# Optimization experiments

Measured on AMD Instinct MI355X. Metric: run time of the kernel, lower is better.

The kernel has to match this reference:

```python
import jax, jax.numpy as jnp
import numpy as np

N, E = 50000, 800000
DIN, H, R, HEADS, DH, OUT = 256, 128, 8, 8, 16, 3  # DH = H // HEADS


def setup_inputs() -> dict:
    key = jax.random.key(0)
    ks = jax.random.split(key, 16)
    g = lambda k, shape, fan: jax.random.normal(k, shape, jnp.float32) * np.float32(np.sqrt(2.0 / fan))
    return {
        'x': jax.random.normal(ks[0], (N, DIN), jnp.float32),
        'edge_index': jax.random.randint(ks[1], (2, E), 0, N, jnp.int32),
        'edge_type': jax.random.randint(ks[2], (E,), 0, R, jnp.int32),
        'Wp': g(ks[3], (DIN, H), DIN), 'bp': jnp.zeros((H,), jnp.float32),
        'W1': g(ks[4], (R, H, H), H), 'root1': g(ks[5], (H, H), H), 'b1': jnp.zeros((H,), jnp.float32),
        'W2': g(ks[6], (R, H, H), H), 'root2': g(ks[7], (H, H), H), 'b2': jnp.zeros((H,), jnp.float32),
        'Wg': g(ks[8], (H, HEADS * DH), H), 'att': g(ks[9], (1, HEADS, 2 * DH), 2 * DH),
        'bg': jnp.zeros((HEADS * DH,), jnp.float32),
        'Wf': g(ks[10], (H, OUT), H), 'bf': jnp.zeros((OUT,), jnp.float32),
    }


def _rgcn(h, src, tgt, etype, W, root, b):
    # h: [N,H]; per-relation: mean-aggregate W_r @ h_src over edges of type r
    n = h.shape[0]
    h_src = h[src]                                   # [E,H]
    out = h @ root
    for r in range(R):
        mask = (etype == r)
        msg = jnp.where(mask[:, None], h_src @ W[r], 0.0)          # [E,H]
        agg = jax.ops.segment_sum(msg, tgt, num_segments=n)        # [N,H]
        deg = jax.ops.segment_sum(mask.astype(h.dtype), tgt, num_segments=n)
        out = out + agg / jnp.clip(deg, 1.0)[:, None]
    return out + b


def _gat(h, src, tgt, Wg, att, bg, negative_slope=0.2):
    n = h.shape[0]
    z = (h @ Wg).reshape(n, HEADS, DH)               # [N,heads,dh]
    z_src, z_tgt = z[src], z[tgt]                    # [E,heads,dh]
    alpha = (z_src * att[:, :, :DH]).sum(-1) + (z_tgt * att[:, :, DH:]).sum(-1)  # [E,heads]
    alpha = jax.nn.leaky_relu(alpha, negative_slope)
    amax = jax.ops.segment_max(alpha, tgt, num_segments=n)         # [N,heads]
    ex = jnp.exp(alpha - amax[tgt])
    denom = jnp.clip(jax.ops.segment_sum(ex, tgt, num_segments=n), 1e-16)
    alpha = ex / denom[tgt]
    out = jax.ops.segment_sum(z_src * alpha[:, :, None], tgt, num_segments=n)  # [N,heads,dh]
    return out.reshape(n, HEADS * DH) + bg


def reference(x, edge_index, edge_type, Wp, bp, W1, root1, b1, W2, root2, b2, Wg, att, bg, Wf, bf):
    src, tgt = edge_index[0], edge_index[1]
    h = x @ Wp + bp
    h = jax.nn.relu(_rgcn(h, src, tgt, edge_type, W1, root1, b1))
    h = jax.nn.relu(_rgcn(h, src, tgt, edge_type, W2, root2, b2))
    h = _gat(h, src, tgt, Wg, att, bg)
    logits = h @ Wf + bf
    return jax.nn.log_softmax(logits, axis=-1)
```

## Files before the change

kernel.cpp:

```cpp
#include <hip/hip_runtime.h>
#include <math.h>

#define NN      50000
#define EE      800000
#define DIN     256
#define HF      128
#define RR      8
#define NHEADS  8
#define DHH     16
#define OUTC    3
#define M2      (NN * RR)
#define NB2     ((M2 + 255) / 256)
#define CH2     ((NB2 + 255) / 256)

static inline int cdiv(long long a, int b) { return (int)((a + b - 1) / b); }

typedef __attribute__((ext_vector_type(8))) short short8;
typedef __attribute__((ext_vector_type(4))) float f32x4;

__device__ inline float bf2f(unsigned short u) {
    return __uint_as_float(((unsigned)u) << 16);
}
__device__ inline unsigned short f2bf(float f) {
    unsigned u = __float_as_uint(f);
    u += 0x7fffu + ((u >> 16) & 1u);
    return (unsigned short)(u >> 16);
}

__global__ __launch_bounds__(256) void prep_weights(const float* __restrict__ Wp,
                                                    const float* __restrict__ W1,
                                                    const float* __restrict__ root1,
                                                    const float* __restrict__ W2,
                                                    const float* __restrict__ root2,
                                                    const float* __restrict__ Wg,
                                                    unsigned short* __restrict__ Wtp_hi,
                                                    unsigned short* __restrict__ Wtp_lo,
                                                    unsigned short* __restrict__ Wt1_hi,
                                                    unsigned short* __restrict__ Wt1_lo,
                                                    unsigned short* __restrict__ Wt2_hi,
                                                    unsigned short* __restrict__ Wt2_lo,
                                                    unsigned short* __restrict__ Wtg_hi,
                                                    unsigned short* __restrict__ Wtg_lo) {
    int i = blockIdx.x * 256 + threadIdx.x;
    if (i >= 344064) return;
    const float* src; unsigned short *dh, *dl; int k0, ldk, base;
    if (i < 32768)       { src = Wp;    dh = Wtp_hi; dl = Wtp_lo; k0 = 0;    ldk = 256;  base = 0; }
    else if (i < 163840) { src = W1;    dh = Wt1_hi; dl = Wt1_lo; k0 = 0;    ldk = 1152; base = 32768; }
    else if (i < 180224) { src = root1; dh = Wt1_hi; dl = Wt1_lo; k0 = 1024; ldk = 1152; base = 163840; }
    else if (i < 311296) { src = W2;    dh = Wt2_hi; dl = Wt2_lo; k0 = 0;    ldk = 1152; base = 180224; }
    else if (i < 327680) { src = root2; dh = Wt2_hi; dl = Wt2_lo; k0 = 1024; ldk = 1152; base = 311296; }
    else                 { src = Wg;    dh = Wtg_hi; dl = Wtg_lo; k0 = 0;    ldk = 128;  base = 327680; }
    int j = i - base;
    int k = j >> 7, n = j & 127;
    float f = src[(size_t)k * 128 + n];
    unsigned short hi = f2bf(f);
    unsigned short lo = f2bf(f - bf2f(hi));
    dh[(size_t)n * ldk + k0 + k] = hi;
    dl[(size_t)n * ldk + k0 + k] = lo;
}

__global__ __launch_bounds__(256) void count2_kernel(const int* __restrict__ tgt,
                                                     const int* __restrict__ et,
                                                     int* __restrict__ cnt2) {
    int i = blockIdx.x * 256 + threadIdx.x;
    if (i < EE) atomicAdd(&cnt2[tgt[i] * RR + et[i]], 1);
}

__global__ __launch_bounds__(256) void scan1_kernel(const int* __restrict__ cnt,
                                                    int* __restrict__ bsum, int n) {
    __shared__ int s[256];
    int t = threadIdx.x;
    int i = blockIdx.x * 256 + t;
    s[t] = (i < n) ? cnt[i] : 0;
    __syncthreads();
    for (int off = 128; off > 0; off >>= 1) {
        if (t < off) s[t] += s[t + off];
        __syncthreads();
    }
    if (t == 0) bsum[blockIdx.x] = s[0];
// ... 137 lines not shown
        *reinterpret_cast<uint4*>(&Bh[srow * APAD + spart]) = rvbh;
        *reinterpret_cast<uint4*>(&Bl[srow * APAD + spart]) = rvbl;
    };

    const int NT = K / BK;
    load_t(0); write_t(); __syncthreads();
    for (int t = 0; t < NT; t++) {
        if (t + 1 < NT) load_t((t + 1) * BK);

        short8 ah[4], al[4];
#pragma unroll
        for (int tt = 0; tt < 4; tt++) {
            ah[tt] = *reinterpret_cast<const short8*>(&Ah[(wr * 64 + tt * 16 + lrow) * APAD + q * 8]);
            if (SPLITA)
                al[tt] = *reinterpret_cast<const short8*>(&Al[(wr * 64 + tt * 16 + lrow) * APAD + q * 8]);
        }
#pragma unroll
        for (int cc = 0; cc < 2; cc++) {
            int cb = wc * 2 + cc;
            short8 bh = *reinterpret_cast<const short8*>(&Bh[(cb * 16 + lrow) * APAD + q * 8]);
            short8 bl = *reinterpret_cast<const short8*>(&Bl[(cb * 16 + lrow) * APAD + q * 8]);
#pragma unroll
            for (int tt = 0; tt < 4; tt++) {
                acc[tt][cc] = __builtin_amdgcn_mfma_f32_16x16x32_bf16(ah[tt], bl, acc[tt][cc], 0, 0, 0);
                if (SPLITA)
                    acc[tt][cc] = __builtin_amdgcn_mfma_f32_16x16x32_bf16(al[tt], bh, acc[tt][cc], 0, 0, 0);
                acc[tt][cc] = __builtin_amdgcn_mfma_f32_16x16x32_bf16(ah[tt], bh, acc[tt][cc], 0, 0, 0);
            }
        }
        __syncthreads();
        if (t + 1 < NT) { write_t(); __syncthreads(); }
    }

#pragma unroll
    for (int t = 0; t < 4; t++) {
#pragma unroll
        for (int r = 0; r < 4; r++) {
            int gmo = m0 + wr * 64 + t * 16 + q * 4 + r;
            if (gmo >= M) continue;
#pragma unroll
            for (int cc = 0; cc < 2; cc++) {
                int gn = (wc * 2 + cc) * 16 + lrow;
                float v = acc[t][cc][r];
                if (BIAS) v += bias[gn];
                if (ACC)  v += C[(size_t)gmo * HF + gn];
                if (RELU) v = fmaxf(v, 0.f);
                C[(size_t)gmo * HF + gn] = v;
                if (BF16OUT) Cb[(size_t)gmo * HF + gn] = f2bf(v);
            }
        }
    }
}

__global__ __launch_bounds__(512) void gemm_rgcn(const unsigned short* __restrict__ aggb,
                                                 const float* __restrict__ hin,
                                                 const unsigned short* __restrict__ Bthi,
                                                 const unsigned short* __restrict__ Btlo,
                                                 float* __restrict__ hout,
                                                 unsigned short* __restrict__ hbout,
                                                 const float* __restrict__ bias, int M) {
    const int LDK = (RR + 1) * HF;
    __shared__ unsigned short Ah[128 * APAD];
    __shared__ unsigned short Al[128 * APAD];
    __shared__ unsigned short Bh[128 * APAD];
    __shared__ unsigned short Bl[128 * APAD];
    const int tid  = threadIdx.x;
    const int m0   = blockIdx.x * 128;
    const int wr   = (tid >> 6) >> 2;
    const int wc   = (tid >> 6) & 3;
    const int lane = tid & 63;
    const int lrow = lane & 15;
    const int q    = lane >> 4;

    f32x4 acc[4][2];
#pragma unroll
    for (int t = 0; t < 4; t++)
#pragma unroll
        for (int c = 0; c < 2; c++) acc[t][c] = (f32x4){0.f, 0.f, 0.f, 0.f};

    const int srow  = tid >> 2;
    const int spart = (tid & 3) * 8;
    const int gm    = m0 + srow;

    uint4 rva1 = make_uint4(0u, 0u, 0u, 0u);
    float rva2[8];
    uint4 rvbh, rvbl;

    auto load1 = [&](int k0) {
        rva1 = make_uint4(0u, 0u, 0u, 0u);
        if (gm < M) rva1 = *reinterpret_cast<const uint4*>(&aggb[(size_t)gm * (RR * HF) + k0 + spart]);
        rvbh = *reinterpret_cast<const uint4*>(&Bthi[(size_t)srow * LDK + k0 + spart]);
        rvbl = *reinterpret_cast<const uint4*>(&Btlo[(size_t)srow * LDK + k0 + spart]);
    };
    auto write1 = [&]() {
        *reinterpret_cast<uint4*>(&Ah[srow * APAD + spart]) = rva1;
        *reinterpret_cast<uint4*>(&Bh[srow * APAD + spart]) = rvbh;
        *reinterpret_cast<uint4*>(&Bl[srow * APAD + spart]) = rvbl;
    };
    auto load2 = [&](int k0) {
        if (gm < M) {
            const float* ap = &hin[(size_t)gm * HF + k0 + spart];
            float4 v0 = *reinterpret_cast<const float4*>(ap);
            float4 v1 = *reinterpret_cast<const float4*>(ap + 4);
            rva2[0] = v0.x; rva2[1] = v0.y; rva2[2] = v0.z; rva2[3] = v0.w;
            rva2[4] = v1.x; rva2[5] = v1.y; rva2[6] = v1.z; rva2[7] = v1.w;
        } else {
#pragma unroll
            for (int j = 0; j < 8; j++) rva2[j] = 0.f;
        }
        rvbh = *reinterpret_cast<const uint4*>(&Bthi[(size_t)srow * LDK + RR * HF + k0 + spart]);
        rvbl = *reinterpret_cast<const uint4*>(&Btlo[(size_t)srow * LDK + RR * HF + k0 + spart]);
    };
    auto write2 = [&]() {
        unsigned hw[4], lw[4];
#pragma unroll
        for (int j = 0; j < 4; j++) {
            unsigned short h0 = f2bf(rva2[2 * j]);
            unsigned short h1 = f2bf(rva2[2 * j + 1]);
            unsigned short l0 = f2bf(rva2[2 * j] - bf2f(h0));
            unsigned short l1 = f2bf(rva2[2 * j + 1] - bf2f(h1));
            hw[j] = (unsigned)h0 | ((unsigned)h1 << 16);
            lw[j] = (unsigned)l0 | ((unsigned)l1 << 16);
        }
        *reinterpret_cast<uint4*>(&Ah[srow * APAD + spart]) = make_uint4(hw[0], hw[1], hw[2], hw[3]);
        *reinterpret_cast<uint4*>(&Al[srow * APAD + spart]) = make_uint4(lw[0], lw[1], lw[2], lw[3]);
        *reinterpret_cast<uint4*>(&Bh[srow * APAD + spart]) = rvbh;
        *reinterpret_cast<uint4*>(&Bl[srow * APAD + spart]) = rvbl;
    };

    load1(0); write1(); __syncthreads();
    for (int t = 0; t < 32; t++) {
        if (t < 31) load1((t + 1) * BK);
        else        load2(0);

        short8 ah[4];
#pragma unroll
        for (int tt = 0; tt < 4; tt++)
            ah[tt] = *reinterpret_cast<const short8*>(&Ah[(wr * 64 + tt * 16 + lrow) * APAD + q * 8]);
#pragma unroll
        for (int cc = 0; cc < 2; cc++) {
            int cb = wc * 2 + cc;
            short8 bh = *reinterpret_cast<const short8*>(&Bh[(cb * 16 + lrow) * APAD + q * 8]);
            short8 bl = *reinterpret_cast<const short8*>(&Bl[(cb * 16 + lrow) * APAD + q * 8]);
#pragma unroll
            for (int tt = 0; tt < 4; tt++) {
                acc[tt][cc] = __builtin_amdgcn_mfma_f32_16x16x32_bf16(ah[tt], bl, acc[tt][cc], 0, 0, 0);
                acc[tt][cc] = __builtin_amdgcn_mfma_f32_16x16x32_bf16(ah[tt], bh, acc[tt][cc], 0, 0, 0);
            }
        }
        __syncthreads();
        if (t < 31) write1(); else write2();
        __syncthreads();
    }

    for (int t = 0; t < 4; t++) {
        if (t < 3) load2((t + 1) * BK);

        short8 ah[4], al[4];
#pragma unroll
        for (int tt = 0; tt < 4; tt++) {
            ah[tt] = *reinterpret_cast<const short8*>(&Ah[(wr * 64 + tt * 16 + lrow) * APAD + q * 8]);
            al[tt] = *reinterpret_cast<const short8*>(&Al[(wr * 64 + tt * 16 + lrow) * APAD + q * 8]);
        }
#pragma unroll
        for (int cc = 0; cc < 2; cc++) {
            int cb = wc * 2 + cc;
            short8 bh = *reinterpret_cast<const short8*>(&Bh[(cb * 16 + lrow) * APAD + q * 8]);
            short8 bl = *reinterpret_cast<const short8*>(&Bl[(cb * 16 + lrow) * APAD + q * 8]);
#pragma unroll
            for (int tt = 0; tt < 4; tt++) {
                acc[tt][cc] = __builtin_amdgcn_mfma_f32_16x16x32_bf16(ah[tt], bl, acc[tt][cc], 0, 0, 0);
                acc[tt][cc] = __builtin_amdgcn_mfma_f32_16x16x32_bf16(al[tt], bh, acc[tt][cc], 0, 0, 0);
                acc[tt][cc] = __builtin_amdgcn_mfma_f32_16x16x32_bf16(ah[tt], bh, acc[tt][cc], 0, 0, 0);
            }
        }
        if (t < 3) {
            __syncthreads();
            write2();
            __syncthreads();
        }
    }

#pragma unroll
    for (int t = 0; t < 4; t++) {
#pragma unroll
        for (int r = 0; r < 4; r++) {
            int gmo = m0 + wr * 64 + t * 16 + q * 4 + r;
            if (gmo >= M) continue;
#pragma unroll
            for (int cc = 0; cc < 2; cc++) {
                int gn = (wc * 2 + cc) * 16 + lrow;
                float v = fmaxf(acc[t][cc][r] + bias[gn], 0.f);
                hout[(size_t)gmo * HF + gn] = v;
                hbout[(size_t)gmo * HF + gn] = f2bf(v);
            }
        }
    }
}

__global__ __launch_bounds__(256) void gemm_z(const float* __restrict__ hin,
                                              const unsigned short* __restrict__ Bthi,
                                              const unsigned short* __restrict__ Btlo,
                                              const float* __restrict__ att,
                                              unsigned short* __restrict__ zb,
                                              float* __restrict__ a_src,
                                              float* __restrict__ a_tgt, int M) {
    __shared__ unsigned short Ah[128 * APAD];
    __shared__ unsigned short Al[128 * APAD];
    __shared__ unsigned short Bh[128 * APAD];
    __shared__ unsigned short Bl[128 * APAD];
    const int tid  = threadIdx.x;
    const int m0   = blockIdx.x * 128;
    const int w    = tid >> 6;
    const int lane = tid & 63;
    const int lrow = lane & 15;
    const int q    = lane >> 4;

    f32x4 acc[2][8];
#pragma unroll
    for (int t = 0; t < 2; t++)
#pragma unroll
        for (int c = 0; c < 8; c++) acc[t][c] = (f32x4){0.f, 0.f, 0.f, 0.f};

    const int srow  = tid >> 1;
    const int spart = (tid & 1) * 16;

    for (int k0 = 0; k0 < HF; k0 += BK) {
        {
            int gm = m0 + srow;
            float va[16];
            if (gm < M) {
                const float* ap = &hin[(size_t)gm * HF + k0 + spart];
#pragma unroll
                for (int j = 0; j < 4; j++) {
                    float4 v = *reinterpret_cast<const float4*>(ap + j * 4);
                    va[j * 4 + 0] = v.x; va[j * 4 + 1] = v.y; va[j * 4 + 2] = v.z; va[j * 4 + 3] = v.w;
                }
            } else {
#pragma unroll
                for (int j = 0; j < 16; j++) va[j] = 0.f;
            }
            unsigned hw[8], lw[8];
#pragma unroll
            for (int j = 0; j < 8; j++) {
                unsigned short h0 = f2bf(va[2 * j]);
// ... 19 lines not shown
        __syncthreads();
        short8 ah[2], al[2];
#pragma unroll
        for (int t = 0; t < 2; t++) {
            ah[t] = *reinterpret_cast<const short8*>(&Ah[(w * 32 + t * 16 + lrow) * APAD + q * 8]);
            al[t] = *reinterpret_cast<const short8*>(&Al[(w * 32 + t * 16 + lrow) * APAD + q * 8]);
        }
#pragma unroll
        for (int c = 0; c < 8; c++) {
            short8 bh = *reinterpret_cast<const short8*>(&Bh[(c * 16 + lrow) * APAD + q * 8]);
            short8 bl = *reinterpret_cast<const short8*>(&Bl[(c * 16 + lrow) * APAD + q * 8]);
#pragma unroll
            for (int t = 0; t < 2; t++) {
                acc[t][c] = __builtin_amdgcn_mfma_f32_16x16x32_bf16(ah[t], bl, acc[t][c], 0, 0, 0);
                acc[t][c] = __builtin_amdgcn_mfma_f32_16x16x32_bf16(al[t], bh, acc[t][c], 0, 0, 0);
                acc[t][c] = __builtin_amdgcn_mfma_f32_16x16x32_bf16(ah[t], bh, acc[t][c], 0, 0, 0);
            }
        }
        __syncthreads();
    }

    float att_s[8], att_t[8];
#pragma unroll
    for (int c = 0; c < 8; c++) {
        att_s[c] = att[c * 32 + lrow];
        att_t[c] = att[c * 32 + 16 + lrow];
    }

#pragma unroll
    for (int t = 0; t < 2; t++) {
#pragma unroll
        for (int r = 0; r < 4; r++) {
            int gm = m0 + w * 32 + t * 16 + q * 4 + r;
            if (gm >= M) continue;
#pragma unroll
            for (int c = 0; c < 8; c++) {
                int gn = c * 16 + lrow;
                float v = acc[t][c][r];
                zb[(size_t)gm * HF + gn] = f2bf(v);
                float ps = v * att_s[c];
                float pt = v * att_t[c];
#pragma unroll
                for (int off = 1; off < 16; off <<= 1) {
                    ps += __shfl_xor(ps, off);
                    pt += __shfl_xor(pt, off);
                }
                if (lrow == 0) {
                    a_src[(size_t)gm * NHEADS + c] = ps;
                    a_tgt[(size_t)gm * NHEADS + c] = pt;
                }
            }
        }
    }
}

__device__ inline void acc8(float* a, uint4 v) {
    a[0] += bf2f((unsigned short)(v.x & 0xffffu));
    a[1] += bf2f((unsigned short)(v.x >> 16));
    a[2] += bf2f((unsigned short)(v.y & 0xffffu));
    a[3] += bf2f((unsigned short)(v.y >> 16));
    a[4] += bf2f((unsigned short)(v.z & 0xffffu));
    a[5] += bf2f((unsigned short)(v.z >> 16));
    a[6] += bf2f((unsigned short)(v.w & 0xffffu));
    a[7] += bf2f((unsigned short)(v.w >> 16));
}

__global__ __launch_bounds__(256) void rgcn_agg_sorted(const unsigned short* __restrict__ hb,
                                                       const int* __restrict__ rowptr2,
                                                       const int* __restrict__ csr_src2,
                                                       unsigned short* __restrict__ agg) {
    int w = (blockIdx.x * 256 + threadIdx.x) >> 6;
    if (w >= NN) return;
    int lane = threadIdx.x & 63;
    int r    = lane >> 3;
    int cg   = (lane & 7) * 16;
    int b8   = w * RR;

    int rp  = rowptr2[b8 + (lane < 9 ? lane : 8)];
    int beg = __shfl(rp, r);
    int end = __shfl(rp, r + 1);

    float a[16];
#pragma unroll
    for (int j = 0; j < 16; j++) a[j] = 0.f;

    int e = beg;
    for (; e + 1 < end; e += 2) {
        int s0 = csr_src2[e];
        int s1 = csr_src2[e + 1];
        const uint4* p0 = reinterpret_cast<const uint4*>(&hb[(size_t)s0 * HF + cg]);
        const uint4* p1 = reinterpret_cast<const uint4*>(&hb[(size_t)s1 * HF + cg]);
        uint4 v00 = p0[0];
        uint4 v01 = p0[1];
        uint4 v10 = p1[0];
        uint4 v11 = p1[1];
        acc8(a,     v00);
        acc8(a + 8, v01);
        acc8(a,     v10);
        acc8(a + 8, v11);
    }
    if (e < end) {
        int s0 = csr_src2[e];
        const uint4* p0 = reinterpret_cast<const uint4*>(&hb[(size_t)s0 * HF + cg]);
        uint4 v00 = p0[0];
        uint4 v01 = p0[1];
        acc8(a,     v00);
        acc8(a + 8, v01);
    }

    int n = end - beg;
    float inv = 1.f / (float)(n > 1 ? n : 1);
    unsigned ow[8];
#pragma unroll
    for (int j = 0; j < 8; j++) {
        ow[j] = (unsigned)f2bf(a[2 * j] * inv) | ((unsigned)f2bf(a[2 * j + 1] * inv) << 16);
    }
    unsigned short* o = &agg[(size_t)w * (RR * HF) + r * HF + cg];
    *reinterpret_cast<uint4*>(o)     = make_uint4(ow[0], ow[1], ow[2], ow[3]);
    *reinterpret_cast<uint4*>(o + 8) = make_uint4(ow[4], ow[5], ow[6], ow[7]);
}

__global__ __launch_bounds__(256) void gat_kernel(const int* __restrict__ rowptr2,
                                                  const int* __restrict__ csr_src2,
                                                  const float* __restrict__ a_src,
                                                  const float* __restrict__ a_tgt,
                                                  const unsigned short* __restrict__ zb,
                                                  const float* __restrict__ bg,
                                                  const float* __restrict__ Wf,
                                                  const float* __restrict__ bf,
                                                  float* __restrict__ out) {
    int w = (blockIdx.x * 256 + threadIdx.x) >> 6;
    if (w >= NN) return;
    int lane = threadIdx.x & 63;
    int beg = rowptr2[w * RR], end = rowptr2[w * RR + RR];

    int hdA = lane & 7;
    int e8  = lane >> 3;
    float atA = a_tgt[w * NHEADS + hdA];
    float m = -1e30f;
    for (int e = beg + e8; e < end; e += 8) {
        int s = csr_src2[e];
        float a = a_src[s * NHEADS + hdA] + atA;
        a = a > 0.f ? a : 0.2f * a;
        m = fmaxf(m, a);
    }
    m = fmaxf(m, __shfl_xor(m, 8));
    m = fmaxf(m, __shfl_xor(m, 16));
    m = fmaxf(m, __shfl_xor(m, 32));

    int half = lane >> 5;
    int l32  = lane & 31;
    int hd   = l32 >> 2;
    int c0   = l32 * 4;

    float l = 0.f;
    float ax0 = 0.f, ax1 = 0.f, ax2 = 0.f, ax3 = 0.f;

    for (int e0 = beg; e0 < end; e0 += 8) {
        int eA = e0 + e8;
        float wA = 0.f;
        int   sA = 0;
        if (eA < end) {
            sA = csr_src2[eA];
            float a = a_src[sA * NHEADS + hdA] + atA;
            a = a > 0.f ? a : 0.2f * a;
            wA = __expf(a - m);
        }
#pragma unroll
        for (int j = 0; j < 4; j++) {
            int idx  = (2 * j + half) * 8 + hd;
            float wv = __shfl(wA, idx);
            int   sv = __shfl(sA, idx);
// ... 14 lines not shown
    float inv = 1.f / fmaxf(l, 1e-16f);
    float v0 = ax0 * inv + bg[c0];
    float v1 = ax1 * inv + bg[c0 + 1];
    float v2 = ax2 * inv + bg[c0 + 2];
    float v3 = ax3 * inv + bg[c0 + 3];

    float p0 = v0 * Wf[c0 * 3 + 0] + v1 * Wf[(c0 + 1) * 3 + 0]
             + v2 * Wf[(c0 + 2) * 3 + 0] + v3 * Wf[(c0 + 3) * 3 + 0];
    float p1 = v0 * Wf[c0 * 3 + 1] + v1 * Wf[(c0 + 1) * 3 + 1]
             + v2 * Wf[(c0 + 2) * 3 + 1] + v3 * Wf[(c0 + 3) * 3 + 1];
    float p2 = v0 * Wf[c0 * 3 + 2] + v1 * Wf[(c0 + 1) * 3 + 2]
             + v2 * Wf[(c0 + 2) * 3 + 2] + v3 * Wf[(c0 + 3) * 3 + 2];
#pragma unroll
    for (int off = 16; off > 0; off >>= 1) {
        p0 += __shfl_xor(p0, off);
        p1 += __shfl_xor(p1, off);
        p2 += __shfl_xor(p2, off);
    }
    if (lane == 0) {
        float l0v = p0 + bf[0], l1v = p1 + bf[1], l2v = p2 + bf[2];
        float mm = fmaxf(l0v, fmaxf(l1v, l2v));
        float lse = mm + logf(expf(l0v - mm) + expf(l1v - mm) + expf(l2v - mm));
        out[(size_t)w * 3 + 0] = l0v - lse;
        out[(size_t)w * 3 + 1] = l1v - lse;
        out[(size_t)w * 3 + 2] = l2v - lse;
    }
}

extern "C" void kernel_launch(void* const* d_in, const int* in_sizes, int n_in,
                              void* d_out, int out_size, void* d_ws, size_t ws_size,
                              hipStream_t stream) {
    const float* x     = (const float*)d_in[0];
    const int*   ei    = (const int*)d_in[1];
    const int*   etype = (const int*)d_in[2];
    const float* Wp    = (const float*)d_in[3];
    const float* bp    = (const float*)d_in[4];
    const float* W1    = (const float*)d_in[5];
    const float* root1 = (const float*)d_in[6];
    const float* b1    = (const float*)d_in[7];
    const float* W2    = (const float*)d_in[8];
    const float* root2 = (const float*)d_in[9];
    const float* b2    = (const float*)d_in[10];
    const float* Wg    = (const float*)d_in[11];
    const float* att   = (const float*)d_in[12];
    const float* bg    = (const float*)d_in[13];
    const float* Wf    = (const float*)d_in[14];
    const float* bf    = (const float*)d_in[15];
    (void)in_sizes; (void)n_in; (void)out_size; (void)ws_size;

    const int* srcv = ei;
    const int* tgtv = ei + EE;

    char* base = (char*)d_ws;
    unsigned short* aggb = (unsigned short*)(base + 0);
    int* cnt2    = (int*)(base + 96000000);
    int* cursor2 = (int*)(base + 98000000);
    int* bsum2   = (int*)(base + 99700000);
    int* bbase2  = (int*)(base + 99800000);
    unsigned short* zb = (unsigned short*)(base + 0);
    float* a_src = (float*)(base + 12800000);
    float* a_tgt = (float*)(base + 14400000);
    float* h1    = (float*)(base + 102400000);
    float* h2    = (float*)(base + 128000000);
    unsigned short* h1b = (unsigned short*)(base + 153600000);
    unsigned short* h2b = (unsigned short*)(base + 166400000);
    int* csr_src2 = (int*)(base + 179200000);
    int* rowptr2  = (int*)(base + 182400000);
    unsigned short* Wtp_hi = (unsigned short*)(base + 184000016);
    unsigned short* Wtp_lo = (unsigned short*)(base + 184065552);
    unsigned short* Wt1_hi = (unsigned short*)(base + 184131088);
    unsigned short* Wt1_lo = (unsigned short*)(base + 184426000);
    unsigned short* Wt2_hi = (unsigned short*)(base + 184720912);
    unsigned short* Wt2_lo = (unsigned short*)(base + 185015824);
    unsigned short* Wtg_hi = (unsigned short*)(base + 185310736);
    unsigned short* Wtg_lo = (unsigned short*)(base + 185343504);

    prep_weights<<<cdiv(344064, 256), 256, 0, stream>>>(
        Wp, W1, root1, W2, root2, Wg,
        Wtp_hi, Wtp_lo, Wt1_hi, Wt1_lo, Wt2_hi, Wt2_lo, Wtg_hi, Wtg_lo);

    hipMemsetAsync(cnt2, 0, (size_t)M2 * 4, stream);
    count2_kernel<<<cdiv(EE, 256), 256, 0, stream>>>(tgtv, etype, cnt2);
    scan1_kernel<<<NB2, 256, 0, stream>>>(cnt2, bsum2, M2);
    scan2_kernel<<<1, 256, 0, stream>>>(bsum2, bbase2, &rowptr2[M2], NB2, CH2);
    scan3_kernel<<<NB2, 256, 0, stream>>>(cnt2, bbase2, rowptr2, cursor2, M2);
    fill2_kernel<<<cdiv(EE, 256), 256, 0, stream>>>(srcv, tgtv, etype, cursor2, csr_src2);

    const int ggrid  = cdiv(NN, 128);
    const int nwgrid = cdiv(NN, 4);

    gemm_mfma<true, false, true, false, true><<<ggrid, 512, 0, stream>>>(
        x, DIN, Wtp_hi, Wtp_lo, DIN, h1, h1b, bp, NN, DIN);

    rgcn_agg_sorted<<<nwgrid, 256, 0, stream>>>(h1b, rowptr2, csr_src2, aggb);
    gemm_rgcn<<<ggrid, 512, 0, stream>>>(aggb, h1, Wt1_hi, Wt1_lo, h2, h2b, b1, NN);

    rgcn_agg_sorted<<<nwgrid, 256, 0, stream>>>(h2b, rowptr2, csr_src2, aggb);
    gemm_rgcn<<<ggrid, 512, 0, stream>>>(aggb, h2, Wt2_hi, Wt2_lo, h1, h1b, b2, NN);

    gemm_z<<<ggrid, 256, 0, stream>>>(h1, Wtg_hi, Wtg_lo, att, zb, a_src, a_tgt, NN);
    gat_kernel<<<nwgrid, 256, 0, stream>>>(rowptr2, csr_src2, a_src, a_tgt, zb, bg, Wf, bf, (float*)d_out);
}
```

Before: 482.3 us.

## Split RGCN GEMM into 128x64 output tiles with 256-thread blocks

The fused RGCN GEMM now gives each block a 128x64 output tile instead of 128x128, using 4 waves of 256 threads, and the grid is doubled so the two column halves run as separate blocks. The two K-phases (bf16 aggregated features, then the split hi/lo fp32 root term) are merged into one loop with unified load and write helpers. This raises the block count (about 391 to 782) for better CU occupancy and cuts shared memory per block. In exchange, each block re-reads the large A operand (aggb), doubling global A traffic, which may already be the dominant cost.

Result: slower. 551.3 us (+14.3%).

```diff
diff --git a/kernel.cpp b/kernel.cpp
--- a/kernel.cpp
+++ b/kernel.cpp
@@ -268,7 +268,7 @@
     }
 }
 
-__global__ __launch_bounds__(512) void gemm_rgcn(const unsigned short* __restrict__ aggb,
+__global__ __launch_bounds__(256) void gemm_rgcn(const unsigned short* __restrict__ aggb,
                                                  const float* __restrict__ hin,
                                                  const unsigned short* __restrict__ Bthi,
                                                  const unsigned short* __restrict__ Btlo,
@@ -278,135 +278,139 @@
     const int LDK = (RR + 1) * HF;
     __shared__ unsigned short Ah[128 * APAD];
     __shared__ unsigned short Al[128 * APAD];
-    __shared__ unsigned short Bh[128 * APAD];
-    __shared__ unsigned short Bl[128 * APAD];
+    __shared__ unsigned short Bh[64 * APAD];
+    __shared__ unsigned short Bl[64 * APAD];
     const int tid  = threadIdx.x;
-    const int m0   = blockIdx.x * 128;
-    const int wr   = (tid >> 6) >> 2;
-    const int wc   = (tid >> 6) & 3;
+    const int bm   = blockIdx.x >> 1;
+    const int bn   = blockIdx.x & 1;
+    const int m0   = bm * 128;
+    const int n0   = bn * 64;
+    const int w    = tid >> 6;
     const int lane = tid & 63;
     const int lrow = lane & 15;
     const int q    = lane >> 4;
 
-    f32x4 acc[4][2];
-#pragma unroll
-    for (int t = 0; t < 4; t++)
-#pragma unroll
-        for (int c = 0; c < 2; c++) acc[t][c] = (f32x4){0.f, 0.f, 0.f, 0.f};
-
-    const int srow  = tid >> 2;
-    const int spart = (tid & 3) * 8;
-    const int gm    = m0 + srow;
-
-    uint4 rva1 = make_uint4(0u, 0u, 0u, 0u);
-    float rva2[8];
+    f32x4 acc[2][4];
+#pragma unroll
+    for (int t = 0; t < 2; t++)
+#pragma unroll
+        for (int c = 0; c < 4; c++) acc[t][c] = (f32x4){0.f, 0.f, 0.f, 0.f};
+
+    const int srowA  = tid >> 1;
+    const int spartA = (tid & 1) * 16;
+    const int srowB  = tid >> 2;
+    const int spartB = (tid & 3) * 8;
+    const int gmA    = m0 + srowA;
+
+    uint4 rvaA0 = make_uint4(0u,0u,0u,0u), rvaA1 = make_uint4(0u,0u,0u,0u);
+    float rva2[16];
     uint4 rvbh, rvbl;
 
-    auto load1 = [&](int k0) {
-        rva1 = make_uint4(0u, 0u, 0u, 0u);
-        if (gm < M) rva1 = *reinterpret_cast<const uint4*>(&aggb[(size_t)gm * (RR * HF) + k0 + spart]);
-        rvbh = *reinterpret_cast<const uint4*>(&Bthi[(size_t)srow * LDK + k0 + spart]);
-        rvbl = *reinterpret_cast<const uint4*>(&Btlo[(size_t)srow * LDK + k0 + spart]);
+    auto load_t = [&](int t) {
+        int k0 = t * BK;
+        if (t < 32) {
+            rvaA0 = make_uint4(0u,0u,0u,0u);
+            rvaA1 = make_uint4(0u,0u,0u,0u);
+            if (gmA < M) {
+                const unsigned short* ap = &aggb[(size_t)gmA * (RR * HF) + k0 + spartA];
+                rvaA0 = *reinterpret_cast<const uint4*>(ap);
+                rvaA1 = *reinterpret_cast<const uint4*>(ap + 8);
+            }
+        } else {
+            int k2 = k0 - RR * HF;
+            if (gmA < M) {
+                const float* ap = &hin[(size_t)gmA * HF + k2 + spartA];
+#pragma unroll
+                for (int j = 0; j < 4; j++) {
+                    float4 v = *reinterpret_cast<const float4*>(ap + j * 4);
+                    rva2[j * 4 + 0] = v.x; rva2[j * 4 + 1] = v.y;
+                    rva2[j * 4 + 2] = v.z; rva2[j * 4 + 3] = v.w;
+                }
+            } else {
+#pragma unroll
+                for (int j = 0; j < 16; j++) rva2[j] = 0.f;
+            }
+        }
+        rvbh = *reinterpret_cast<const uint4*>(&Bthi[(size_t)(n0 + srowB) * LDK + k0 + spartB]);
+        rvbl = *reinterpret_cast<const uint4*>(&Btlo[(size_t)(n0 + srowB) * LDK + k0 + spartB]);
     };
-    auto write1 = [&]() {
-        *reinterpret_cast<uint4*>(&Ah[srow * APAD + spart]) = rva1;
-        *reinterpret_cast<uint4*>(&Bh[srow * APAD + spart]) = rvbh;
-        *reinterpret_cast<uint4*>(&Bl[srow * APAD + spart]) = rvbl;
+    auto write_t = [&](int t) {
+        if (t < 32) {
+            *reinterpret_cast<uint4*>(&Ah[srowA * APAD + spartA])     = rvaA0;
+            *reinterpret_cast<uint4*>(&Ah[srowA * APAD + spartA + 8]) = rvaA1;
+        } else {
+            unsigned hw[8], lw[8];
+#pragma unroll
+            for (int j = 0; j < 8; j++) {
+                unsigned short h0 = f2bf(rva2[2 * j]);
+                unsigned short h1 = f2bf(rva2[2 * j + 1]);
+                unsigned short l0 = f2bf(rva2[2 * j] - bf2f(h0));
+                unsigned short l1 = f2bf(rva2[2 * j + 1] - bf2f(h1));
+                hw[j] = (unsigned)h0 | ((unsigned)h1 << 16);
+                lw[j] = (unsigned)l0 | ((unsigned)l1 << 16);
+            }
+            *reinterpret_cast<uint4*>(&Ah[srowA * APAD + spartA])     = make_uint4(hw[0], hw[1], hw[2], hw[3]);
+            *reinterpret_cast<uint4*>(&Ah[srowA * APAD + spartA + 8]) = make_uint4(hw[4], hw[5], hw[6], hw[7]);
+            *reinterpret_cast<uint4*>(&Al[srowA * APAD + spartA])     = make_uint4(lw[0], lw[1], lw[2], lw[3]);
+            *reinterpret_cast<uint4*>(&Al[srowA * APAD + spartA + 8]) = make_uint4(lw[4], lw[5], lw[6], lw[7]);
+        }
+        *reinterpret_cast<uint4*>(&Bh[srowB * APAD + spartB]) = rvbh;
+        *reinterpret_cast<uint4*>(&Bl[srowB * APAD + spartB]) = rvbl;
     };
-    auto load2 = [&](int k0) {
-        if (gm < M) {
-            const float* ap = &hin[(size_t)gm * HF + k0 + spart];
-            float4 v0 = *reinterpret_cast<const float4*>(ap);
-            float4 v1 = *reinterpret_cast<const float4*>(ap + 4);
-            rva2[0] = v0.x; rva2[1] = v0.y; rva2[2] = v0.z; rva2[3] = v0.w;
-            rva2[4] = v1.x; rva2[5] = v1.y; rva2[6] = v1.z; rva2[7] = v1.w;
+
+    const int NT = LDK / BK;
+    load_t(0); write_t(0); __syncthreads();
+    for (int t = 0; t < NT; t++) {
+        if (t + 1 < NT) load_t(t + 1);
+
+        if (t < 32) {
+            short8 ah[2];
+#pragma unroll
+            for (int tt = 0; tt < 2; tt++)
+                ah[tt] = *reinterpret_cast<const short8*>(&Ah[(w * 32 + tt * 16 + lrow) * APAD + q * 8]);
+#pragma unroll
+            for (int cc = 0; cc < 4; cc++) {
+                short8 bh = *reinterpret_cast<const short8*>(&Bh[(cc * 16 + lrow) * APAD + q * 8]);
+                short8 bl = *reinterpret_cast<const short8*>(&Bl[(cc * 16 + lrow) * APAD + q * 8]);
+#pragma unroll
+                for (int tt = 0; tt < 2; tt++) {
+                    acc[tt][cc] = __builtin_amdgcn_mfma_f32_16x16x32_bf16(ah[tt], bl, acc[tt][cc], 0, 0, 0);
+                    acc[tt][cc] = __builtin_amdgcn_mfma_f32_16x16x32_bf16(ah[tt], bh, acc[tt][cc], 0, 0, 0);
+                }
+            }
         } else {
-#pragma unroll
-            for (int j = 0; j < 8; j++) rva2[j] = 0.f;
-        }
-        rvbh = *reinterpret_cast<const uint4*>(&Bthi[(size_t)srow * LDK + RR * HF + k0 + spart]);
-        rvbl = *reinterpret_cast<const uint4*>(&Btlo[(size_t)srow * LDK + RR * HF + k0 + spart]);
-    };
-    auto write2 = [&]() {
-        unsigned hw[4], lw[4];
-#pragma unroll
-        for (int j = 0; j < 4; j++) {
-            unsigned short h0 = f2bf(rva2[2 * j]);
-            unsigned short h1 = f2bf(rva2[2 * j + 1]);
-            unsigned short l0 = f2bf(rva2[2 * j] - bf2f(h0));
-            unsigned short l1 = f2bf(rva2[2 * j + 1] - bf2f(h1));
-            hw[j] = (unsigned)h0 | ((unsigned)h1 << 16);
-            lw[j] = (unsigned)l0 | ((unsigned)l1 << 16);
-        }
-        *reinterpret_cast<uint4*>(&Ah[srow * APAD + spart]) = make_uint4(hw[0], hw[1], hw[2], hw[3]);
-        *reinterpret_cast<uint4*>(&Al[srow * APAD + spart]) = make_uint4(lw[0], lw[1], lw[2], lw[3]);
-        *reinterpret_cast<uint4*>(&Bh[srow * APAD + spart]) = rvbh;
-        *reinterpret_cast<uint4*>(&Bl[srow * APAD + spart]) = rvbl;
-    };
-
-    load1(0); write1(); __syncthreads();
-    for (int t = 0; t < 32; t++) {
-        if (t < 31) load1((t + 1) * BK);
-        else        load2(0);
-
-        short8 ah[4];
-#pragma unroll
-        for (int tt = 0; tt < 4; tt++)
-            ah[tt] = *reinterpret_cast<const short8*>(&Ah[(wr * 64 + tt * 16 + lrow) * APAD + q * 8]);
-#pragma unroll
-        for (int cc = 0; cc < 2; cc++) {
-            int cb = wc * 2 + cc;
-            short8 bh = *reinterpret_cast<const short8*>(&Bh[(cb * 16 + lrow) * APAD + q * 8]);
-            short8 bl = *reinterpret_cast<const short8*>(&Bl[(cb * 16 + lrow) * APAD + q * 8]);
-#pragma unroll
-            for (int tt = 0; tt < 4; tt++) {
-                acc[tt][cc] = __builtin_amdgcn_mfma_f32_16x16x32_bf16(ah[tt], bl, acc[tt][cc], 0, 0, 0);
-                acc[tt][cc] = __builtin_amdgcn_mfma_f32_16x16x32_bf16(ah[tt], bh, acc[tt][cc], 0, 0, 0);
-            }
-        }
-        __syncthreads();
-        if (t < 31) write1(); else write2();
-        __syncthreads();
-    }
-
-    for (int t = 0; t < 4; t++) {
-        if (t < 3) load2((t + 1) * BK);
-
-        short8 ah[4], al[4];
-#pragma unroll
-        for (int tt = 0; tt < 4; tt++) {
-            ah[tt] = *reinterpret_cast<const short8*>(&Ah[(wr * 64 + tt * 16 + lrow) * APAD + q * 8]);
-            al[tt] = *reinterpret_cast<const short8*>(&Al[(wr * 64 + tt * 16 + lrow) * APAD + q * 8]);
-        }
-#pragma unroll
-        for (int cc = 0; cc < 2; cc++) {
-            int cb = wc * 2 + cc;
-            short8 bh = *reinterpret_cast<const short8*>(&Bh[(cb * 16 + lrow) * APAD + q * 8]);
-            short8 bl = *reinterpret_cast<const short8*>(&Bl[(cb * 16 + lrow) * APAD + q * 8]);
-#pragma unroll
-            for (int tt = 0; tt < 4; tt++) {
-                acc[tt][cc] = __builtin_amdgcn_mfma_f32_16x16x32_bf16(ah[tt], bl, acc[tt][cc], 0, 0, 0);
-                acc[tt][cc] = __builtin_amdgcn_mfma_f32_16x16x32_bf16(al[tt], bh, acc[tt][cc], 0, 0, 0);
-                acc[tt][cc] = __builtin_amdgcn_mfma_f32_16x16x32_bf16(ah[tt], bh, acc[tt][cc], 0, 0, 0);
-            }
-        }
-        if (t < 3) {
-            __syncthreads();
-            write2();
-            __syncthreads();
-        }
-    }
-
-#pragma unroll
-    for (int t = 0; t < 4; t++) {
+            short8 ah[2], al[2];
+#pragma unroll
+            for (int tt = 0; tt < 2; tt++) {
+                ah[tt] = *reinterpret_cast<const short8*>(&Ah[(w * 32 + tt * 16 + lrow) * APAD + q * 8]);
+                al[tt] = *reinterpret_cast<const short8*>(&Al[(w * 32 + tt * 16 + lrow) * APAD + q * 8]);
+            }
+#pragma unroll
+            for (int cc = 0; cc < 4; cc++) {
+                short8 bh = *reinterpret_cast<const short8*>(&Bh[(cc * 16 + lrow) * APAD + q * 8]);
+                short8 bl = *reinterpret_cast<const short8*>(&Bl[(cc * 16 + lrow) * APAD + q * 8]);
+#pragma unroll
+                for (int tt = 0; tt < 2; tt++) {
+                    acc[tt][cc] = __builtin_amdgcn_mfma_f32_16x16x32_bf16(ah[tt], bl, acc[tt][cc], 0, 0, 0);
+                    acc[tt][cc] = __builtin_amdgcn_mfma_f32_16x16x32_bf16(al[tt], bh, acc[tt][cc], 0, 0, 0);
+                    acc[tt][cc] = __builtin_amdgcn_mfma_f32_16x16x32_bf16(ah[tt], bh, acc[tt][cc], 0, 0, 0);
+                }
+            }
+        }
+        __syncthreads();
+        if (t + 1 < NT) { write_t(t + 1); __syncthreads(); }
+    }
+
+#pragma unroll
+    for (int tt = 0; tt < 2; tt++) {
 #pragma unroll
         for (int r = 0; r < 4; r++) {
-            int gmo = m0 + wr * 64 + t * 16 + q * 4 + r;
+            int gmo = m0 + w * 32 + tt * 16 + q * 4 + r;
             if (gmo >= M) continue;
 #pragma unroll
-            for (int cc = 0; cc < 2; cc++) {
-                int gn = (wc * 2 + cc) * 16 + lrow;
-                float v = fmaxf(acc[t][cc][r] + bias[gn], 0.f);
+            for (int cc = 0; cc < 4; cc++) {
+                int gn = n0 + cc * 16 + lrow;
+                float v = fmaxf(acc[tt][cc][r] + bias[gn], 0.f);
                 hout[(size_t)gmo * HF + gn] = v;
                 hbout[(size_t)gmo * HF + gn] = f2bf(v);
             }
@@ -759,10 +763,10 @@
         x, DIN, Wtp_hi, Wtp_lo, DIN, h1, h1b, bp, NN, DIN);
 
     rgcn_agg_sorted<<<nwgrid, 256, 0, stream>>>(h1b, rowptr2, csr_src2, aggb);
-    gemm_rgcn<<<ggrid, 512, 0, stream>>>(aggb, h1, Wt1_hi, Wt1_lo, h2, h2b, b1, NN);
+    gemm_rgcn<<<ggrid * 2, 256, 0, stream>>>(aggb, h1, Wt1_hi, Wt1_lo, h2, h2b, b1, NN);
 
     rgcn_agg_sorted<<<nwgrid, 256, 0, stream>>>(h2b, rowptr2, csr_src2, aggb);
-    gemm_rgcn<<<ggrid, 512, 0, stream>>>(aggb, h2, Wt2_hi, Wt2_lo, h1, h1b, b2, NN);
+    gemm_rgcn<<<ggrid * 2, 256, 0, stream>>>(aggb, h2, Wt2_hi, Wt2_lo, h1, h1b, b2, NN);
 
     gemm_z<<<ggrid, 256, 0, stream>>>(h1, Wtg_hi, Wtg_lo, att, zb, a_src, a_tgt, NN);
     gat_kernel<<<nwgrid, 256, 0, stream>>>(rowptr2, csr_src2, a_src, a_tgt, zb, bg, Wf, bf, (float*)d_out);
```

## Fuse RGCN neighbor aggregation into the MFMA GEMM kernel via shared memory

Applied to the files above, without the earlier changes.

Replaces the separate rgcn_agg_sorted kernel and gemm_rgcn kernel with a single fused_rgcn kernel. Each block aggregates the per-relation mean of neighbor features for its 128 rows directly into shared memory, one relation at a time, and feeds that tile to the MFMA loop. This removes the write and read of the large [N, R*H] bf16 aggregate buffer in global memory and one launch per layer. In exchange, the gather is done by only 512 threads per 128 rows, each holding 32 float accumulators, and it is serialized with the MFMA work behind barriers. That can lower memory-level parallelism, raise register pressure, and add shared memory use that may reduce occupancy.

Measured after the change: 560.4 us. 16.2% more time.

```diff
diff --git a/kernel.cpp b/kernel.cpp
--- a/kernel.cpp
+++ b/kernel.cpp
@@ -25,6 +25,16 @@
     unsigned u = __float_as_uint(f);
     u += 0x7fffu + ((u >> 16) & 1u);
     return (unsigned short)(u >> 16);
+}
+__device__ inline void acc8(float* a, uint4 v) {
+    a[0] += bf2f((unsigned short)(v.x & 0xffffu));
+    a[1] += bf2f((unsigned short)(v.x >> 16));
+    a[2] += bf2f((unsigned short)(v.y & 0xffffu));
+    a[3] += bf2f((unsigned short)(v.y >> 16));
+    a[4] += bf2f((unsigned short)(v.z & 0xffffu));
+    a[5] += bf2f((unsigned short)(v.z >> 16));
+    a[6] += bf2f((unsigned short)(v.w & 0xffffu));
+    a[7] += bf2f((unsigned short)(v.w >> 16));
 }
 
 __global__ __launch_bounds__(256) void prep_weights(const float* __restrict__ Wp,
@@ -268,16 +278,19 @@
     }
 }
 
-__global__ __launch_bounds__(512) void gemm_rgcn(const unsigned short* __restrict__ aggb,
-                                                 const float* __restrict__ hin,
-                                                 const unsigned short* __restrict__ Bthi,
-                                                 const unsigned short* __restrict__ Btlo,
-                                                 float* __restrict__ hout,
-                                                 unsigned short* __restrict__ hbout,
-                                                 const float* __restrict__ bias, int M) {
+__global__ __launch_bounds__(512) void fused_rgcn(const unsigned short* __restrict__ hb,
+                                                  const float* __restrict__ hin,
+                                                  const int* __restrict__ rowptr2,
+                                                  const int* __restrict__ csr_src2,
+                                                  const unsigned short* __restrict__ Bthi,
+                                                  const unsigned short* __restrict__ Btlo,
+                                                  float* __restrict__ hout,
+                                                  unsigned short* __restrict__ hbout,
+                                                  const float* __restrict__ bias, int M) {
     const int LDK = (RR + 1) * HF;
-    __shared__ unsigned short Ah[128 * APAD];
-    __shared__ unsigned short Al[128 * APAD];
+    __shared__ unsigned short Agg[4][128 * APAD];
+    __shared__ unsigned short A2h[128 * APAD];
+    __shared__ unsigned short A2l[128 * APAD];
     __shared__ unsigned short Bh[128 * APAD];
     __shared__ unsigned short Bl[128 * APAD];
     const int tid  = threadIdx.x;
@@ -296,63 +309,129 @@
 
     const int srow  = tid >> 2;
     const int spart = (tid & 3) * 8;
+    const int tc    = tid & 3;
     const int gm    = m0 + srow;
 
-    uint4 rva1 = make_uint4(0u, 0u, 0u, 0u);
     float rva2[8];
     uint4 rvbh, rvbl;
 
-    auto load1 = [&](int k0) {
-        rva1 = make_uint4(0u, 0u, 0u, 0u);
-        if (gm < M) rva1 = *reinterpret_cast<const uint4*>(&aggb[(size_t)gm * (RR * HF) + k0 + spart]);
+    auto load_t = [&](int t) {
+        int k0 = t * BK;
+        if (t >= 32) {
+            int k2 = k0 - RR * HF;
+            if (gm < M) {
+                const float* ap = &hin[(size_t)gm * HF + k2 + spart];
+                float4 v0 = *reinterpret_cast<const float4*>(ap);
+                float4 v1 = *reinterpret_cast<const float4*>(ap + 4);
+                rva2[0] = v0.x; rva2[1] = v0.y; rva2[2] = v0.z; rva2[3] = v0.w;
+                rva2[4] = v1.x; rva2[5] = v1.y; rva2[6] = v1.z; rva2[7] = v1.w;
+            } else {
+#pragma unroll
+                for (int j = 0; j < 8; j++) rva2[j] = 0.f;
+            }
+        }
         rvbh = *reinterpret_cast<const uint4*>(&Bthi[(size_t)srow * LDK + k0 + spart]);
         rvbl = *reinterpret_cast<const uint4*>(&Btlo[(size_t)srow * LDK + k0 + spart]);
     };
-    auto write1 = [&]() {
-        *reinterpret_cast<uint4*>(&Ah[srow * APAD + spart]) = rva1;
+    auto write_t = [&](int t) {
+        if (t >= 32) {
+            unsigned hw[4], lw[4];
+#pragma unroll
+            for (int j = 0; j < 4; j++) {
+                unsigned short h0 = f2bf(rva2[2 * j]);
+                unsigned short h1 = f2bf(rva2[2 * j + 1]);
+                unsigned short l0 = f2bf(rva2[2 * j] - bf2f(h0));
+                unsigned short l1 = f2bf(rva2[2 * j + 1] - bf2f(h1));
+                hw[j] = (unsigned)h0 | ((unsigned)h1 << 16);
+                lw[j] = (unsigned)l0 | ((unsigned)l1 << 16);
+            }
+            *reinterpret_cast<uint4*>(&A2h[srow * APAD + spart]) = make_uint4(hw[0], hw[1], hw[2], hw[3]);
+            *reinterpret_cast<uint4*>(&A2l[srow * APAD + spart]) = make_uint4(lw[0], lw[1], lw[2], lw[3]);
+        }
         *reinterpret_cast<uint4*>(&Bh[srow * APAD + spart]) = rvbh;
         *reinterpret_cast<uint4*>(&Bl[srow * APAD + spart]) = rvbl;
     };
-    auto load2 = [&](int k0) {
+
+    auto agg_phase = [&](int r) {
+        float a[32];
+#pragma unroll
+        for (int j = 0; j < 32; j++) a[j] = 0.f;
+        int beg = 0, end = 0;
         if (gm < M) {
-            const float* ap = &hin[(size_t)gm * HF + k0 + spart];
-            float4 v0 = *reinterpret_cast<const float4*>(ap);
-            float4 v1 = *reinterpret_cast<const float4*>(ap + 4);
-            rva2[0] = v0.x; rva2[1] = v0.y; rva2[2] = v0.z; rva2[3] = v0.w;
-            rva2[4] = v1.x; rva2[5] = v1.y; rva2[6] = v1.z; rva2[7] = v1.w;
-        } else {
-#pragma unroll
-            for (int j = 0; j < 8; j++) rva2[j] = 0.f;
-        }
-        rvbh = *reinterpret_cast<const uint4*>(&Bthi[(size_t)srow * LDK + RR * HF + k0 + spart]);
-        rvbl = *reinterpret_cast<const uint4*>(&Btlo[(size_t)srow * LDK + RR * HF + k0 + spart]);
+            beg = rowptr2[gm * RR + r];
+            end = rowptr2[gm * RR + r + 1];
+        }
+        int e = beg;
+        for (; e + 1 < end; e += 2) {
+            int s0 = csr_src2[e];
+            int s1 = csr_src2[e + 1];
+            const uint4* p0 = reinterpret_cast<const uint4*>(&hb[(size_t)s0 * HF + tc * 32]);
+            const uint4* p1 = reinterpret_cast<const uint4*>(&hb[(size_t)s1 * HF + tc * 32]);
+            uint4 v00 = p0[0], v01 = p0[1], v02 = p0[2], v03 = p0[3];
+            uint4 v10 = p1[0], v11 = p1[1], v12 = p1[2], v13 = p1[3];
+            acc8(a,      v00); acc8(a + 8,  v01); acc8(a + 16, v02); acc8(a + 24, v03);
+            acc8(a,      v10); acc8(a + 8,  v11); acc8(a + 16, v12); acc8(a + 24, v13);
+        }
+        if (e < end) {
+            int s0 = csr_src2[e];
+            const uint4* p0 = reinterpret_cast<const uint4*>(&hb[(size_t)s0 * HF + tc * 32]);
+            uint4 v00 = p0[0], v01 = p0[1], v02 = p0[2], v03 = p0[3];
+            acc8(a, v00); acc8(a + 8, v01); acc8(a + 16, v02); acc8(a + 24, v03);
+        }
+        int n = end - beg;
+        float inv = 1.f / (float)(n > 1 ? n : 1);
+        unsigned ow[16];
+#pragma unroll
+        for (int j = 0; j < 16; j++)
+            ow[j] = (unsigned)f2bf(a[2 * j] * inv) | ((unsigned)f2bf(a[2 * j + 1] * inv) << 16);
+        unsigned short* o = &Agg[tc][srow * APAD];
+        *reinterpret_cast<uint4*>(o)      = make_uint4(ow[0],  ow[1],  ow[2],  ow[3]);
+        *reinterpret_cast<uint4*>(o + 8)  = make_uint4(ow[4],  ow[5],  ow[6],  ow[7]);
+        *reinterpret_cast<uint4*>(o + 16) = make_uint4(ow[8],  ow[9],  ow[10], ow[11]);
+        *reinterpret_cast<uint4*>(o + 24) = make_uint4(ow[12], ow[13], ow[14], ow[15]);
     };
-    auto write2 = [&]() {
-        unsigned hw[4], lw[4];
-#pragma unroll
-        for (int j = 0; j < 4; j++) {
-            unsigned short h0 = f2bf(rva2[2 * j]);
-            unsigned short h1 = f2bf(rva2[2 * j + 1]);
-            unsigned short l0 = f2bf(rva2[2 * j] - bf2f(h0));
-            unsigned short l1 = f2bf(rva2[2 * j + 1] - bf2f(h1));
-            hw[j] = (unsigned)h0 | ((unsigned)h1 << 16);
-            lw[j] = (unsigned)l0 | ((unsigned)l1 << 16);
-        }
-        *reinterpret_cast<uint4*>(&Ah[srow * APAD + spart]) = make_uint4(hw[0], hw[1], hw[2], hw[3]);
-        *reinterpret_cast<uint4*>(&Al[srow * APAD + spart]) = make_uint4(lw[0], lw[1], lw[2], lw[3]);
-        *reinterpret_cast<uint4*>(&Bh[srow * APAD + spart]) = rvbh;
-        *reinterpret_cast<uint4*>(&Bl[srow * APAD + spart]) = rvbl;
-    };
-
-    load1(0); write1(); __syncthreads();
-    for (int t = 0; t < 32; t++) {
-        if (t < 31) load1((t + 1) * BK);
-        else        load2(0);
-
-        short8 ah[4];
-#pragma unroll
-        for (int tt = 0; tt < 4; tt++)
-            ah[tt] = *reinterpret_cast<const short8*>(&Ah[(wr * 64 + tt * 16 + lrow) * APAD + q * 8]);
+
+    load_t(0); write_t(0);
+    for (int r = 0; r < RR; r++) {
+        agg_phase(r);
+        __syncthreads();
+#pragma unroll
+        for (int kc = 0; kc < 4; kc++) {
+            int t = r * 4 + kc;
+            if (t + 1 < 36) load_t(t + 1);
+
+            short8 ah[4];
+#pragma unroll
+            for (int tt = 0; tt < 4; tt++)
+                ah[tt] = *reinterpret_cast<const short8*>(
+                    &Agg[kc][(wr * 64 + tt * 16 + lrow) * APAD + q * 8]);
+#pragma unroll
+            for (int cc = 0; cc < 2; cc++) {
+                int cb = wc * 2 + cc;
+                short8 bh = *reinterpret_cast<const short8*>(&Bh[(cb * 16 + lrow) * APAD + q * 8]);
+                short8 bl = *reinterpret_cast<const short8*>(&Bl[(cb * 16 + lrow) * APAD + q * 8]);
+#pragma unroll
+                for (int tt = 0; tt < 4; tt++) {
+                    acc[tt][cc] = __builtin_amdgcn_mfma_f32_16x16x32_bf16(ah[tt], bl, acc[tt][cc], 0, 0, 0);
+                    acc[tt][cc] = __builtin_amdgcn_mfma_f32_16x16x32_bf16(ah[tt], bh, acc[tt][cc], 0, 0, 0);
+                }
+            }
+            __syncthreads();
+            if (t + 1 < 36) write_t(t + 1);
+            if (kc < 3) __syncthreads();
+        }
+    }
+
+    __syncthreads();
+    for (int t = 32; t < 36; t++) {
+        if (t + 1 < 36) load_t(t + 1);
+
+        short8 ah[4], al[4];
+#pragma unroll
+        for (int tt = 0; tt < 4; tt++) {
+            ah[tt] = *reinterpret_cast<const short8*>(&A2h[(wr * 64 + tt * 16 + lrow) * APAD + q * 8]);
+            al[tt] = *reinterpret_cast<const short8*>(&A2l[(wr * 64 + tt * 16 + lrow) * APAD + q * 8]);
+        }
 #pragma unroll
         for (int cc = 0; cc < 2; cc++) {
             int cb = wc * 2 + cc;
@@ -361,40 +440,12 @@
 #pragma unroll
             for (int tt = 0; tt < 4; tt++) {
                 acc[tt][cc] = __builtin_amdgcn_mfma_f32_16x16x32_bf16(ah[tt], bl, acc[tt][cc], 0, 0, 0);
-                acc[tt][cc] = __builtin_amdgcn_mfma_f32_16x16x32_bf16(ah[tt], bh, acc[tt][cc], 0, 0, 0);
-            }
-        }
-        __syncthreads();
-        if (t < 31) write1(); else write2();
-        __syncthreads();
-    }
-
-    for (int t = 0; t < 4; t++) {
-        if (t < 3) load2((t + 1) * BK);
-
-        short8 ah[4], al[4];
-#pragma unroll
-        for (int tt = 0; tt < 4; tt++) {
-            ah[tt] = *reinterpret_cast<const short8*>(&Ah[(wr * 64 + tt * 16 + lrow) * APAD + q * 8]);
-            al[tt] = *reinterpret_cast<const short8*>(&Al[(wr * 64 + tt * 16 + lrow) * APAD + q * 8]);
-        }
-#pragma unroll
-        for (int cc = 0; cc < 2; cc++) {
-            int cb = wc * 2 + cc;
-            short8 bh = *reinterpret_cast<const short8*>(&Bh[(cb * 16 + lrow) * APAD + q * 8]);
-            short8 bl = *reinterpret_cast<const short8*>(&Bl[(cb * 16 + lrow) * APAD + q * 8]);
-#pragma unroll
-            for (int tt = 0; tt < 4; tt++) {
-                acc[tt][cc] = __builtin_amdgcn_mfma_f32_16x16x32_bf16(ah[tt], bl, acc[tt][cc], 0, 0, 0);
                 acc[tt][cc] = __builtin_amdgcn_mfma_f32_16x16x32_bf16(al[tt], bh, acc[tt][cc], 0, 0, 0);
                 acc[tt][cc] = __builtin_amdgcn_mfma_f32_16x16x32_bf16(ah[tt], bh, acc[tt][cc], 0, 0, 0);
             }
         }
-        if (t < 3) {
-            __syncthreads();
-            write2();
-            __syncthreads();
-        }
+        __syncthreads();
+        if (t + 1 < 36) { write_t(t + 1); __syncthreads(); }
     }
 
 #pragma unroll
@@ -532,72 +583,6 @@
             }
         }
     }
-}
-
-__device__ inline void acc8(float* a, uint4 v) {
-    a[0] += bf2f((unsigned short)(v.x & 0xffffu));
-    a[1] += bf2f((unsigned short)(v.x >> 16));
-    a[2] += bf2f((unsigned short)(v.y & 0xffffu));
-    a[3] += bf2f((unsigned short)(v.y >> 16));
-    a[4] += bf2f((unsigned short)(v.z & 0xffffu));
-    a[5] += bf2f((unsigned short)(v.z >> 16));
-    a[6] += bf2f((unsigned short)(v.w & 0xffffu));
-    a[7] += bf2f((unsigned short)(v.w >> 16));
-}
-
-__global__ __launch_bounds__(256) void rgcn_agg_sorted(const unsigned short* __restrict__ hb,
-                                                       const int* __restrict__ rowptr2,
-                                                       const int* __restrict__ csr_src2,
-                                                       unsigned short* __restrict__ agg) {
-    int w = (blockIdx.x * 256 + threadIdx.x) >> 6;
-    if (w >= NN) return;
-    int lane = threadIdx.x & 63;
-    int r    = lane >> 3;
-    int cg   = (lane & 7) * 16;
-    int b8   = w * RR;
-
-    int rp  = rowptr2[b8 + (lane < 9 ? lane : 8)];
-    int beg = __shfl(rp, r);
-    int end = __shfl(rp, r + 1);
-
-    float a[16];
-#pragma unroll
-    for (int j = 0; j < 16; j++) a[j] = 0.f;
-
-    int e = beg;
-    for (; e + 1 < end; e += 2) {
-        int s0 = csr_src2[e];
-        int s1 = csr_src2[e + 1];
-        const uint4* p0 = reinterpret_cast<const uint4*>(&hb[(size_t)s0 * HF + cg]);
-        const uint4* p1 = reinterpret_cast<const uint4*>(&hb[(size_t)s1 * HF + cg]);
-        uint4 v00 = p0[0];
-        uint4 v01 = p0[1];
-        uint4 v10 = p1[0];
-        uint4 v11 = p1[1];
-        acc8(a,     v00);
-        acc8(a + 8, v01);
-        acc8(a,     v10);
-        acc8(a + 8, v11);
-    }
-    if (e < end) {
-        int s0 = csr_src2[e];
-        const uint4* p0 = reinterpret_cast<const uint4*>(&hb[(size_t)s0 * HF + cg]);
-        uint4 v00 = p0[0];
-        uint4 v01 = p0[1];
-        acc8(a,     v00);
-        acc8(a + 8, v01);
-    }
-
-    int n = end - beg;
-    float inv = 1.f / (float)(n > 1 ? n : 1);
-    unsigned ow[8];
-#pragma unroll
-    for (int j = 0; j < 8; j++) {
-        ow[j] = (unsigned)f2bf(a[2 * j] * inv) | ((unsigned)f2bf(a[2 * j + 1] * inv) << 16);
-    }
-    unsigned short* o = &agg[(size_t)w * (RR * HF) + r * HF + cg];
-    *reinterpret_cast<uint4*>(o)     = make_uint4(ow[0], ow[1], ow[2], ow[3]);
-    *reinterpret_cast<uint4*>(o + 8) = make_uint4(ow[4], ow[5], ow[6], ow[7]);
 }
 
 __global__ __launch_bounds__(256) void gat_kernel(const int* __restrict__ rowptr2,
@@ -718,7 +703,6 @@
     const int* tgtv = ei + EE;
 
     char* base = (char*)d_ws;
-    unsigned short* aggb = (unsigned short*)(base + 0);
     int* cnt2    = (int*)(base + 96000000);
     int* cursor2 = (int*)(base + 98000000);
     int* bsum2   = (int*)(base + 99700000);
@@ -758,11 +742,11 @@
     gemm_mfma<true, false, true, false, true><<<ggrid, 512, 0, stream>>>(
         x, DIN, Wtp_hi, Wtp_lo, DIN, h1, h1b, bp, NN, DIN);
 
-    rgcn_agg_sorted<<<nwgrid, 256, 0, stream>>>(h1b, rowptr2, csr_src2, aggb);
-    gemm_rgcn<<<ggrid, 512, 0, stream>>>(aggb, h1, Wt1_hi, Wt1_lo, h2, h2b, b1, NN);
-
-    rgcn_agg_sorted<<<nwgrid, 256, 0, stream>>>(h2b, rowptr2, csr_src2, aggb);
-    gemm_rgcn<<<ggrid, 512, 0, stream>>>(aggb, h2, Wt2_hi, Wt2_lo, h1, h1b, b2, NN);
+    fused_rgcn<<<ggrid, 512, 0, stream>>>(h1b, h1, rowptr2, csr_src2,
+                                          Wt1_hi, Wt1_lo, h2, h2b, b1, NN);
+
+    fused_rgcn<<<ggrid, 512, 0, stream>>>(h2b, h2, rowptr2, csr_src2,
+                                          Wt2_hi, Wt2_lo, h1, h1b, b2, NN);
 
     gemm_z<<<ggrid, 256, 0, stream>>>(h1, Wtg_hi, Wtg_lo, att, zb, a_src, a_tgt, NN);
     gat_kernel<<<nwgrid, 256, 0, stream>>>(rowptr2, csr_src2, a_src, a_tgt, zb, bg, Wf, bf, (float*)d_out);
```
